# Performance work log

Hardware: AMD Instinct MI355X
Metric: run time of the kernel (lower is better)

## Reference

```python
import jax, jax.numpy as jnp
import numpy as np

NUM_EXPERTS = 64
TOPK = 2
N_TOKENS = 16384
DIM = 4096


def setup_inputs() -> dict:
    key = jax.random.key(0)
    k1, k2 = jax.random.split(key)
    x = jax.random.normal(k1, (N_TOKENS, DIM), dtype=jnp.float32)
    # gate weight, torch nn.Linear layout: [num_experts, dim], trunc-normal-ish small init
    W = jax.random.normal(k2, (NUM_EXPERTS, DIM), dtype=jnp.float32) * 0.02
    return {"x": x, "W": W}


def reference(x, W):
    # gate: logits = x @ W^T  -> [N, E]
    router_logits = x @ W.T
    # softmax computed in fp32 (matches dtype=torch.float32 in source)
    routing_weights = jax.nn.softmax(router_logits.astype(jnp.float32), axis=-1)
    # top-k experts per token
    top_w, selected_experts = jax.lax.top_k(routing_weights, TOPK)  # [N, k]
    top_w = top_w.astype(x.dtype)
    sel_flat = selected_experts.reshape(-1)  # [N*k]
    # histogram over experts (torch.histc with bins=num_experts)
    num_tokens_per_expert = jnp.bincount(sel_flat, length=NUM_EXPERTS)
    # stable argsort -> gather (permutation) indices grouping tokens by expert
    gather_indices = jnp.argsort(sel_flat, stable=True)
    return top_w.reshape(-1), gather_indices, num_tokens_per_expert
```

## Files before the change

kernel.cpp:

```cpp
#include <hip/hip_runtime.h>
#include <hip/hip_bf16.h>
#include <math.h>
#include <stdint.h>

#define N_TOKENS 16384
#define DIM 4096
#define NEXP 64

typedef const __attribute__((address_space(1))) void gvoid_t;
typedef __attribute__((address_space(3))) void svoid_t;
typedef short bf16x8 __attribute__((ext_vector_type(8)));
typedef float f32x4 __attribute__((ext_vector_type(4)));

constexpr int TOK_BLK = 16;

__device__ __forceinline__ unsigned short bf16_rn(float f) {
  unsigned u = __float_as_uint(f);
  u += 0x7fffu + ((u >> 16) & 1u);
  return (unsigned short)(u >> 16);
}
__device__ __forceinline__ float bf16_tof(unsigned short h) {
  return __uint_as_float(((unsigned)h) << 16);
}

__device__ __forceinline__ void split8(const float4 a, const float4 b,
                                       bf16x8& hi, bf16x8& lo) {
  const float f[8] = {a.x, a.y, a.z, a.w, b.x, b.y, b.z, b.w};
  union { unsigned u[4]; bf16x8 v; } H, L;
#pragma unroll
  for (int p = 0; p < 4; ++p) {
    const float2 fp = make_float2(f[2 * p], f[2 * p + 1]);
    const __hip_bfloat162 hh = __float22bfloat162_rn(fp);
    const unsigned uh = *(const unsigned*)&hh;
    const float h0 = __uint_as_float(uh << 16);
    const float h1 = __uint_as_float(uh & 0xffff0000u);
    const __hip_bfloat162 ll =
        __float22bfloat162_rn(make_float2(fp.x - h0, fp.y - h1));
    H.u[p] = uh;
    L.u[p] = *(const unsigned*)&ll;
  }
  hi = H.v;
  lo = L.v;
}

__global__ __launch_bounds__(256) void k0_wsplit(const float* __restrict__ W,
                                                 unsigned short* __restrict__ hi,
                                                 unsigned short* __restrict__ lo,
                                                 int* __restrict__ cnt) {
  const int i = (blockIdx.x * 256 + threadIdx.x) * 4;
  const float4 f = *(const float4*)(W + i);
  ushort4 h, l;
  h.x = bf16_rn(f.x); l.x = bf16_rn(f.x - bf16_tof(h.x));
  h.y = bf16_rn(f.y); l.y = bf16_rn(f.y - bf16_tof(h.y));
  h.z = bf16_rn(f.z); l.z = bf16_rn(f.z - bf16_tof(h.z));
  h.w = bf16_rn(f.w); l.w = bf16_rn(f.w - bf16_tof(h.w));
  *(ushort4*)(hi + i) = h;
  *(ushort4*)(lo + i) = l;
  if (blockIdx.x < 8) {
    int4* c4 = (int4*)cnt;
    c4[blockIdx.x * 256 + threadIdx.x] = make_int4(0, 0, 0, 0);
  }
}

__global__ __launch_bounds__(256, 4) void k1_fused(
    const float* __restrict__ x, const unsigned short* __restrict__ Whi,
    const unsigned short* __restrict__ Wlo, float* __restrict__ topw,
    int* __restrict__ sel, int* __restrict__ cnt) {
  __shared__ __align__(16) unsigned char smem[40960];
  float* const x0 = (float*)smem;
  float* const x1 = (float*)(smem + 4096);
  unsigned short* const wh0 = (unsigned short*)(smem + 8192);
  unsigned short* const wh1 = (unsigned short*)(smem + 16384);
  unsigned short* const wl0 = (unsigned short*)(smem + 24576);
  unsigned short* const wl1 = (unsigned short*)(smem + 32768);
  float* const lg = (float*)smem;
  int* const hist = (int*)(smem + 4608);

  const int tid = threadIdx.x;
  const int lane = tid & 63;
  const int wid = __builtin_amdgcn_readfirstlane(tid >> 6);
  const int r = lane & 15;
  const int g = lane >> 4;
  const int tok0 = blockIdx.x * TOK_BLK;

  f32x4 acc = {};

  auto stage = [&](float* xd, unsigned short* whd, unsigned short* wld,
                   int kc) {
    {
      const int r0 = wid * 4;
      const int row = r0 + (lane >> 4);
      const float* src =
          x + (size_t)(tok0 + row) * DIM + kc + 4 * ((lane & 15) ^ (row & 15));
      __builtin_amdgcn_global_load_lds((gvoid_t*)src, (svoid_t*)(xd + r0 * 64),
                                       16, 0, 0);
    }
#pragma unroll
    for (int q = 0; q < 2; ++q) {
      const int r0 = wid * 16 + q * 8;
      const int row = r0 + (lane >> 3);
      const int s = (lane & 7) ^ (row & 7);
      __builtin_amdgcn_global_load_lds(
          (gvoid_t*)(Whi + (size_t)row * DIM + kc + 8 * s),
          (svoid_t*)(whd + r0 * 64), 16, 0, 0);
      __builtin_amdgcn_global_load_lds(
          (gvoid_t*)(Wlo + (size_t)row * DIM + kc + 8 * s),
          (svoid_t*)(wld + r0 * 64), 16, 0, 0);
    }
  };

  auto compute = [&](const float* xb, const unsigned short* whb,
                     const unsigned short* wlb) {
#pragma unroll
    for (int h = 0; h < 2; ++h) {
      const int s0 = h * 8 + 2 * g;
      const float4 fa = *(const float4*)(xb + r * 64 + 4 * (s0 ^ r));
      const float4 fb = *(const float4*)(xb + r * 64 + 4 * ((s0 + 1) ^ r));
      bf16x8 Ahi, Alo;
      split8(fa, fb, Ahi, Alo);
      const int wrow = wid * 16 + r;
      const int wadr = wrow * 64 + 8 * ((h * 4 + g) ^ (wrow & 7));
      const bf16x8 Bhi = *(const bf16x8*)(whb + wadr);
      const bf16x8 Blo = *(const bf16x8*)(wlb + wadr);
      acc = __builtin_amdgcn_mfma_f32_16x16x32_bf16(Ahi, Bhi, acc, 0, 0, 0);
      acc = __builtin_amdgcn_mfma_f32_16x16x32_bf16(Alo, Bhi, acc, 0, 0, 0);
      acc = __builtin_amdgcn_mfma_f32_16x16x32_bf16(Ahi, Blo, acc, 0, 0, 0);
    }
  };

  stage(x0, wh0, wl0, 0);
  for (int t = 0; t < 64; t += 2) {
    if (t + 1 < 64) {
      stage(x1, wh1, wl1, (t + 1) * 64);
      asm volatile("s_waitcnt vmcnt(5)" ::: "memory");
    } else {
      asm volatile("s_waitcnt vmcnt(0)" ::: "memory");
    }
    __builtin_amdgcn_sched_barrier(0);
    __builtin_amdgcn_s_barrier();
    compute(x0, wh0, wl0);
    __builtin_amdgcn_s_barrier();
    __builtin_amdgcn_sched_barrier(0);
    if (t + 2 < 64) {
      stage(x0, wh0, wl0, (t + 2) * 64);
      asm volatile("s_waitcnt vmcnt(5)" ::: "memory");
    } else {
      asm volatile("s_waitcnt vmcnt(0)" ::: "memory");
    }
    __builtin_amdgcn_sched_barrier(0);
    __builtin_amdgcn_s_barrier();
    compute(x1, wh1, wl1);
    __builtin_amdgcn_s_barrier();
    __builtin_amdgcn_sched_barrier(0);
  }

  if (tid < NEXP) hist[tid] = 0;
#pragma unroll
  for (int rg = 0; rg < 4; ++rg)
    lg[(g * 4 + rg) * 68 + wid * 16 + r] = acc[rg];
  __syncthreads();

  if (tid < TOK_BLK) {
    const float* rowp = lg + tid * 68;
    float4 v[16];
#pragma unroll
    for (int c = 0; c < 16; ++c) v[c] = *(const float4*)(rowp + c * 4);

    float v0 = -INFINITY, v1 = -INFINITY;
    int i0 = 0, i1 = 0;
#define TOP2_STEP(val, idx)                                  \
  {                                                          \
    const float vv = (val);                                  \
    const int ee = (idx);                                    \
    if (vv > v0) { v1 = v0; i1 = i0; v0 = vv; i0 = ee; }     \
    else if (vv > v1) { v1 = vv; i1 = ee; }                  \
  }
#pragma unroll
    for (int c = 0; c < 16; ++c) {
      TOP2_STEP(v[c].x, c * 4 + 0);
      TOP2_STEP(v[c].y, c * 4 + 1);
      TOP2_STEP(v[c].z, c * 4 + 2);
      TOP2_STEP(v[c].w, c * 4 + 3);
    }
#undef TOP2_STEP

    float denom = 0.f;
#pragma unroll
    for (int c = 0; c < 16; ++c) {
      denom += expf(v[c].x - v0);
      denom += expf(v[c].y - v0);
      denom += expf(v[c].z - v0);
      denom += expf(v[c].w - v0);
    }
    const float w0s = 1.0f / denom;
    const float w1s = expf(v1 - v0) / denom;

    const int tk = tok0 + tid;
    topw[2 * tk + 0] = w0s;
    topw[2 * tk + 1] = w1s;
    sel[2 * tk + 0] = i0;
    sel[2 * tk + 1] = i1;
    atomicAdd(&hist[i0], 1);
    atomicAdd(&hist[i1], 1);
  }
  __syncthreads();
  if (tid < NEXP) {
    const int h = hist[tid];
    if (h) atomicAdd(&cnt[tid * 128 + (blockIdx.x >> 3)], h);
  }
}

__global__ __launch_bounds__(256) void k4_scatter(const int* __restrict__ cnt,
                                                  const int* __restrict__ sel,
                                                  float* __restrict__ gout,
                                                  float* __restrict__ counts_out) {
  __shared__ int tot[NEXP], parts[NEXP], cbs[NEXP], wcnt[4 * NEXP];
  const int tid = threadIdx.x;
  const int b = blockIdx.x;
  const int s = b * 256 + tid;
  const int e = sel[s];
  const int lane = tid & 63;
  const int wv = tid >> 6;
  wcnt[tid] = 0;

  if (tid < NEXP) {
    const int4* row4 = (const int4*)(cnt + tid * 128);
    int run = 0, part = 0;
#pragma unroll
    for (int q = 0; q < 32; ++q) {
      const int4 v = row4[q];
      if (4 * q + 0 < b) part += v.x;
      if (4 * q + 1 < b) part += v.y;
      if (4 * q + 2 < b) part += v.z;
      if (4 * q + 3 < b) part += v.w;
      run += v.x + v.y + v.z + v.w;
    }
    tot[tid] = run;
    parts[tid] = part;
    if (b == 0) counts_out[tid] = (float)run;
  }
  __syncthreads();
  if (tid < NEXP) {
    int g2 = 0;
    for (int q = 0; q < tid; ++q) g2 += tot[q];
    cbs[tid] = g2 + parts[tid];
  }

  unsigned long long mask = ~0ull;
#pragma unroll
  for (int bb = 0; bb < 6; ++bb) {
    const unsigned long long bl = __ballot((e >> bb) & 1);
    mask &= ((e >> bb) & 1) ? bl : ~bl;
  }
  const unsigned long long below = mask & ((1ull << lane) - 1ull);
  const int wr = __popcll(below);
  if (wr == 0) wcnt[wv * NEXP + e] = __popcll(mask);
  __syncthreads();

  int base = cbs[e];
  for (int w2 = 0; w2 < wv; ++w2) base += wcnt[w2 * NEXP + e];
  gout[base + wr] = (float)s;
}

extern "C" void kernel_launch(void* const* d_in, const int* in_sizes, int n_in,
                              void* d_out, int out_size, void* d_ws, size_t ws_size,
                              hipStream_t stream) {
  const float* x = (const float*)d_in[0];
  const float* W = (const float*)d_in[1];
  float* out = (float*)d_out;

  unsigned short* whi_g = (unsigned short*)d_ws;
  unsigned short* wlo_g = whi_g + NEXP * DIM;
  int* sel = (int*)(wlo_g + NEXP * DIM);
  int* cnt = sel + N_TOKENS * 2;

  hipLaunchKernelGGL(k0_wsplit, dim3((NEXP * DIM) / 1024), dim3(256), 0, stream,
                     W, whi_g, wlo_g, cnt);
  hipLaunchKernelGGL(k1_fused, dim3(N_TOKENS / TOK_BLK), dim3(256), 0, stream,
                     x, whi_g, wlo_g, out, sel, cnt);
  hipLaunchKernelGGL(k4_scatter, dim3((2 * N_TOKENS) / 256), dim3(256), 0, stream,
                     cnt, sel, out + 2 * N_TOKENS,
                     out + 2 * N_TOKENS + 2 * N_TOKENS);
}
```

Baseline: 94.23 us.

## Fuse weight bf16 hi/lo split into main GEMM kernel, drop pre-split pass

```diff
diff --git a/kernel.cpp b/kernel.cpp
--- a/kernel.cpp
+++ b/kernel.cpp
@@ -13,15 +13,6 @@
 typedef float f32x4 __attribute__((ext_vector_type(4)));
 
 constexpr int TOK_BLK = 16;
-
-__device__ __forceinline__ unsigned short bf16_rn(float f) {
-  unsigned u = __float_as_uint(f);
-  u += 0x7fffu + ((u >> 16) & 1u);
-  return (unsigned short)(u >> 16);
-}
-__device__ __forceinline__ float bf16_tof(unsigned short h) {
-  return __uint_as_float(((unsigned)h) << 16);
-}
 
 __device__ __forceinline__ void split8(const float4 a, const float4 b,
                                        bf16x8& hi, bf16x8& lo) {
@@ -43,36 +34,14 @@
   lo = L.v;
 }
 
-__global__ __launch_bounds__(256) void k0_wsplit(const float* __restrict__ W,
-                                                 unsigned short* __restrict__ hi,
-                                                 unsigned short* __restrict__ lo,
-                                                 int* __restrict__ cnt) {
-  const int i = (blockIdx.x * 256 + threadIdx.x) * 4;
-  const float4 f = *(const float4*)(W + i);
-  ushort4 h, l;
-  h.x = bf16_rn(f.x); l.x = bf16_rn(f.x - bf16_tof(h.x));
-  h.y = bf16_rn(f.y); l.y = bf16_rn(f.y - bf16_tof(h.y));
-  h.z = bf16_rn(f.z); l.z = bf16_rn(f.z - bf16_tof(h.z));
-  h.w = bf16_rn(f.w); l.w = bf16_rn(f.w - bf16_tof(h.w));
-  *(ushort4*)(hi + i) = h;
-  *(ushort4*)(lo + i) = l;
-  if (blockIdx.x < 8) {
-    int4* c4 = (int4*)cnt;
-    c4[blockIdx.x * 256 + threadIdx.x] = make_int4(0, 0, 0, 0);
-  }
-}
-
 __global__ __launch_bounds__(256, 4) void k1_fused(
-    const float* __restrict__ x, const unsigned short* __restrict__ Whi,
-    const unsigned short* __restrict__ Wlo, float* __restrict__ topw,
-    int* __restrict__ sel, int* __restrict__ cnt) {
+    const float* __restrict__ x, const float* __restrict__ W,
+    float* __restrict__ topw, int* __restrict__ sel, int* __restrict__ cnt) {
   __shared__ __align__(16) unsigned char smem[40960];
   float* const x0 = (float*)smem;
   float* const x1 = (float*)(smem + 4096);
-  unsigned short* const wh0 = (unsigned short*)(smem + 8192);
-  unsigned short* const wh1 = (unsigned short*)(smem + 16384);
-  unsigned short* const wl0 = (unsigned short*)(smem + 24576);
-  unsigned short* const wl1 = (unsigned short*)(smem + 32768);
+  float* const wf0 = (float*)(smem + 8192);
+  float* const wf1 = (float*)(smem + 24576);
   float* const lg = (float*)smem;
   int* const hist = (int*)(smem + 4608);
 
@@ -85,8 +54,7 @@
 
   f32x4 acc = {};
 
-  auto stage = [&](float* xd, unsigned short* whd, unsigned short* wld,
-                   int kc) {
+  auto stage = [&](float* xd, float* wfd, int kc) {
     {
       const int r0 = wid * 4;
       const int row = r0 + (lane >> 4);
@@ -96,21 +64,17 @@
                                        16, 0, 0);
     }
 #pragma unroll
-    for (int q = 0; q < 2; ++q) {
-      const int r0 = wid * 16 + q * 8;
-      const int row = r0 + (lane >> 3);
-      const int s = (lane & 7) ^ (row & 7);
-      __builtin_amdgcn_global_load_lds(
-          (gvoid_t*)(Whi + (size_t)row * DIM + kc + 8 * s),
-          (svoid_t*)(whd + r0 * 64), 16, 0, 0);
-      __builtin_amdgcn_global_load_lds(
-          (gvoid_t*)(Wlo + (size_t)row * DIM + kc + 8 * s),
-          (svoid_t*)(wld + r0 * 64), 16, 0, 0);
+    for (int q = 0; q < 4; ++q) {
+      const int r0 = wid * 16 + q * 4;
+      const int row = r0 + (lane >> 4);
+      const float* src =
+          W + (size_t)row * DIM + kc + 4 * ((lane & 15) ^ (row & 15));
+      __builtin_amdgcn_global_load_lds((gvoid_t*)src, (svoid_t*)(wfd + r0 * 64),
+                                       16, 0, 0);
     }
   };
 
-  auto compute = [&](const float* xb, const unsigned short* whb,
-                     const unsigned short* wlb) {
+  auto compute = [&](const float* xb, const float* wfb) {
 #pragma unroll
     for (int h = 0; h < 2; ++h) {
       const int s0 = h * 8 + 2 * g;
@@ -119,37 +83,40 @@
       bf16x8 Ahi, Alo;
       split8(fa, fb, Ahi, Alo);
       const int wrow = wid * 16 + r;
-      const int wadr = wrow * 64 + 8 * ((h * 4 + g) ^ (wrow & 7));
-      const bf16x8 Bhi = *(const bf16x8*)(whb + wadr);
-      const bf16x8 Blo = *(const bf16x8*)(wlb + wadr);
+      const float4 wa =
+          *(const float4*)(wfb + wrow * 64 + 4 * (s0 ^ (wrow & 15)));
+      const float4 wb =
+          *(const float4*)(wfb + wrow * 64 + 4 * ((s0 + 1) ^ (wrow & 15)));
+      bf16x8 Bhi, Blo;
+      split8(wa, wb, Bhi, Blo);
       acc = __builtin_amdgcn_mfma_f32_16x16x32_bf16(Ahi, Bhi, acc, 0, 0, 0);
       acc = __builtin_amdgcn_mfma_f32_16x16x32_bf16(Alo, Bhi, acc, 0, 0, 0);
       acc = __builtin_amdgcn_mfma_f32_16x16x32_bf16(Ahi, Blo, acc, 0, 0, 0);
     }
   };
 
-  stage(x0, wh0, wl0, 0);
+  stage(x0, wf0, 0);
   for (int t = 0; t < 64; t += 2) {
     if (t + 1 < 64) {
-      stage(x1, wh1, wl1, (t + 1) * 64);
+      stage(x1, wf1, (t + 1) * 64);
       asm volatile("s_waitcnt vmcnt(5)" ::: "memory");
     } else {
       asm volatile("s_waitcnt vmcnt(0)" ::: "memory");
     }
     __builtin_amdgcn_sched_barrier(0);
     __builtin_amdgcn_s_barrier();
-    compute(x0, wh0, wl0);
+    compute(x0, wf0);
     __builtin_amdgcn_s_barrier();
     __builtin_amdgcn_sched_barrier(0);
     if (t + 2 < 64) {
-      stage(x0, wh0, wl0, (t + 2) * 64);
+      stage(x0, wf0, (t + 2) * 64);
       asm volatile("s_waitcnt vmcnt(5)" ::: "memory");
     } else {
       asm volatile("s_waitcnt vmcnt(0)" ::: "memory");
     }
     __builtin_amdgcn_sched_barrier(0);
     __builtin_amdgcn_s_barrier();
-    compute(x1, wh1, wl1);
+    compute(x1, wf1);
     __builtin_amdgcn_s_barrier();
     __builtin_amdgcn_sched_barrier(0);
   }
@@ -269,15 +236,12 @@
   const float* W = (const float*)d_in[1];
   float* out = (float*)d_out;
 
-  unsigned short* whi_g = (unsigned short*)d_ws;
-  unsigned short* wlo_g = whi_g + NEXP * DIM;
-  int* sel = (int*)(wlo_g + NEXP * DIM);
+  int* sel = (int*)d_ws;
   int* cnt = sel + N_TOKENS * 2;
 
-  hipLaunchKernelGGL(k0_wsplit, dim3((NEXP * DIM) / 1024), dim3(256), 0, stream,
-                     W, whi_g, wlo_g, cnt);
+  hipMemsetAsync(cnt, 0, 128 * NEXP * sizeof(int), stream);
   hipLaunchKernelGGL(k1_fused, dim3(N_TOKENS / TOK_BLK), dim3(256), 0, stream,
-                     x, whi_g, wlo_g, out, sel, cnt);
+                     x, W, out, sel, cnt);
   hipLaunchKernelGGL(k4_scatter, dim3((2 * N_TOKENS) / 256), dim3(256), 0, stream,
                      cnt, sel, out + 2 * N_TOKENS,
                      out + 2 * N_TOKENS + 2 * N_TOKENS);
```

After: 115.5 us. 1.23x slower.
